# Optimization experiments

Hardware: AMD Instinct MI355X
Metric: run time of the kernel (lower is better)

The kernel has to match this reference:

```python
import jax, jax.numpy as jnp
import numpy as np

DIM = 192; HEADS = 6; WS = 7; RES = 56; SHIFT = 3
HEAD_DIM = DIM // HEADS
SCALE = HEAD_DIM ** -0.5
N = WS * WS
EPS = 1e-5

def _rel_pos_index():
    coords = np.stack(np.meshgrid(np.arange(WS), np.arange(WS), indexing='ij')).reshape(2, -1)
    rel = coords[:, :, None] - coords[:, None, :]  # [2,N,N]
    rel = rel.transpose(1, 2, 0)
    rel[:, :, 0] += WS - 1
    rel[:, :, 1] += WS - 1
    rel[:, :, 0] *= 2 * WS - 1
    return rel.sum(-1)  # [N,N]

def _attn_mask():
    img = np.zeros((RES, RES), dtype=np.float32)
    slices = (slice(0, -WS), slice(-WS, -SHIFT), slice(-SHIFT, None))
    cnt = 0
    for h in slices:
        for w in slices:
            img[h, w] = cnt; cnt += 1
    mw = img.reshape(RES // WS, WS, RES // WS, WS).transpose(0, 2, 1, 3).reshape(-1, N)  # [nW,N]
    diff = mw[:, None, :] - mw[:, :, None]
    return np.where(diff != 0, -100.0, 0.0).astype(np.float32)  # [nW,N,N]

REL_IDX = jnp.asarray(_rel_pos_index())
ATTN_MASK = jnp.asarray(_attn_mask())

def _ln(x, g, b):
    mu = x.mean(-1, keepdims=True)
    var = ((x - mu) ** 2).mean(-1, keepdims=True)
    return (x - mu) * jax.lax.rsqrt(var + EPS) * g + b

def setup_inputs() -> dict:
    key = jax.random.key(0)
    ks = jax.random.split(key, 8)
    d = {
        'x': jax.random.normal(ks[0], (32, RES * RES, DIM), jnp.float32),
        'norm1_g': jnp.ones((DIM,), jnp.float32), 'norm1_b': jnp.zeros((DIM,), jnp.float32),
        'qkv_w': jax.random.normal(ks[1], (DIM, 3 * DIM), jnp.float32) * 0.02,
        'qkv_b': jnp.zeros((3 * DIM,), jnp.float32),
        'proj_w': jax.random.normal(ks[2], (DIM, DIM), jnp.float32) * 0.02,
        'proj_b': jnp.zeros((DIM,), jnp.float32),
        'bias_table': jax.random.normal(ks[3], ((2 * WS - 1) ** 2, HEADS), jnp.float32) * 0.02,
        'norm2_g': jnp.ones((DIM,), jnp.float32), 'norm2_b': jnp.zeros((DIM,), jnp.float32),
        'fc1_w': jax.random.normal(ks[4], (DIM, 4 * DIM), jnp.float32) * 0.02,
        'fc1_b': jnp.zeros((4 * DIM,), jnp.float32),
        'fc2_w': jax.random.normal(ks[5], (4 * DIM, DIM), jnp.float32) * 0.02,
        'fc2_b': jnp.zeros((DIM,), jnp.float32),
    }
    return d

def reference(x, norm1_g, norm1_b, qkv_w, qkv_b, proj_w, proj_b, bias_table,
              norm2_g, norm2_b, fc1_w, fc1_b, fc2_w, fc2_b):
    B, L, C = x.shape
    H = W = RES
    shortcut = x
    h = _ln(x, norm1_g, norm1_b).reshape(B, H, W, C)
    # cyclic shift
    h = jnp.roll(h, (-SHIFT, -SHIFT), axis=(1, 2))
    # window partition -> [B*nW, N, C]
    nH = H // WS
    h = h.reshape(B, nH, WS, nH, WS, C).transpose(0, 1, 3, 2, 4, 5).reshape(-1, N, C)
    BW = h.shape[0]
    # windowed MHSA
    qkv = (h @ qkv_w + qkv_b).reshape(BW, N, 3, HEADS, HEAD_DIM)
    q, k, v = qkv[:, :, 0], qkv[:, :, 1], qkv[:, :, 2]  # [BW,N,h,hd]
    attn = jnp.einsum('bnhd,bmhd->bhnm', q, k) * SCALE  # [BW,h,N,N]
    bias = bias_table[REL_IDX.reshape(-1)].reshape(N, N, HEADS).transpose(2, 0, 1)
    attn = attn + bias[None]
    nW = ATTN_MASK.shape[0]
    attn = attn.reshape(BW // nW, nW, HEADS, N, N) + ATTN_MASK[None, :, None]
    attn = jax.nn.softmax(attn.reshape(BW, HEADS, N, N), axis=-1)
    h = jnp.einsum('bhnm,bmhd->bnhd', attn, v).reshape(BW, N, C)
    h = h @ proj_w + proj_b
    # window reverse
    h = h.reshape(B, nH, nH, WS, WS, C).transpose(0, 1, 3, 2, 4, 5).reshape(B, H, W, C)
    h = jnp.roll(h, (SHIFT, SHIFT), axis=(1, 2)).reshape(B, L, C)
    x = shortcut + h
    # MLP
    m = _ln(x, norm2_g, norm2_b)
    m = jax.nn.gelu(m @ fc1_w + fc1_b, approximate=False) @ fc2_w + fc2_b
    return x + m
```

## Files before the change

kernel.cpp:

```cpp
#include <hip/hip_runtime.h>
#include <hip/hip_bf16.h>
#include <math.h>

typedef __attribute__((ext_vector_type(8))) short bh8;
typedef __attribute__((ext_vector_type(4))) short sh4;
typedef __attribute__((ext_vector_type(4))) float fx4;

__device__ __forceinline__ fx4 mfma_bf16(bh8 a, bh8 b, fx4 c) {
    return __builtin_amdgcn_mfma_f32_16x16x32_bf16(a, b, c, 0, 0, 0);
}

__device__ __forceinline__ void gload16(const __hip_bfloat16* g, __hip_bfloat16* l) {
    __builtin_amdgcn_global_load_lds(
        (const __attribute__((address_space(1))) void*)g,
        (__attribute__((address_space(3))) void*)l,
        16, 0, 0);
}

__device__ __forceinline__ float fast_erf(float u) {
    float au = fabsf(u);
    float t  = __builtin_amdgcn_rcpf(1.0f + 0.3275911f * au);
    float p  = ((((1.061405429f * t - 1.453152027f) * t + 1.421413741f) * t
                 - 0.284496736f) * t + 0.254829592f) * t;
    float e  = __expf(-u * u);
    return copysignf(1.0f - p * e, u);
}

#define WAITV6 do { asm volatile("s_waitcnt vmcnt(6)" ::: "memory"); \
                    __builtin_amdgcn_sched_barrier(0); } while (0)
#define WAITV0 do { asm volatile("s_waitcnt vmcnt(0)" ::: "memory"); \
                    __builtin_amdgcn_sched_barrier(0); } while (0)
#define LGKM0  do { asm volatile("s_waitcnt lgkmcnt(0)" ::: "memory"); \
                    __builtin_amdgcn_sched_barrier(0); } while (0)
#define BARR   do { __builtin_amdgcn_s_barrier(); \
                    __builtin_amdgcn_sched_barrier(0); } while (0)

__global__ __launch_bounds__(256)
void convw_k(const float* __restrict__ W, __hip_bfloat16* __restrict__ Wt, int K, int Nn)
{
    int idx = blockIdx.x * 256 + threadIdx.x;
    if (idx < K * Nn) {
        int k = idx / Nn, n = idx - k * Nn;
        Wt[(size_t)n * K + k] = __float2bfloat16(W[idx]);
    }
}

__global__ __launch_bounds__(256)
void ln1_gather_k(const float* __restrict__ x, const float* __restrict__ g,
                  const float* __restrict__ bia, __hip_bfloat16* __restrict__ xw)
{
    const int wave = threadIdx.x >> 6, lane = threadIdx.x & 63;
    const int t = blockIdx.x * 4 + wave;
    const int w = t / 49, n = t - w * 49;
    const int b = w >> 6, wrem = w & 63, wi = wrem >> 3, wj = wrem & 7;
    const int i = n / 7, j = n - i * 7;
    int sr = wi * 7 + i + 3; if (sr >= 56) sr -= 56;
    int sc = wj * 7 + j + 3; if (sc >= 56) sc -= 56;
    const float* xp = x + ((size_t)b * 3136 + sr * 56 + sc) * 192;
    float v0 = xp[lane], v1 = xp[lane + 64], v2 = xp[lane + 128];
    float s = v0 + v1 + v2;
    float q = v0 * v0 + v1 * v1 + v2 * v2;
    for (int off = 32; off > 0; off >>= 1) {
        s += __shfl_down(s, off, 64);
        q += __shfl_down(q, off, 64);
    }
    s = __shfl(s, 0, 64); q = __shfl(q, 0, 64);
    float mean = s * (1.0f / 192.0f);
    float var  = q * (1.0f / 192.0f) - mean * mean;
    float rstd = rsqrtf(var + 1e-5f);
    __hip_bfloat16* op = xw + (size_t)t * 192;
    op[lane]       = __float2bfloat16((v0 - mean) * rstd * g[lane]       + bia[lane]);
    op[lane + 64]  = __float2bfloat16((v1 - mean) * rstd * g[lane + 64]  + bia[lane + 64]);
    op[lane + 128] = __float2bfloat16((v2 - mean) * rstd * g[lane + 128] + bia[lane + 128]);
}

template<int MODE, int K, int NOUT>
__global__ __launch_bounds__(256)
void gemm2_k(const __hip_bfloat16* __restrict__ A,
             const __hip_bfloat16* __restrict__ Bt,
             const float* __restrict__ bias,
             const float* __restrict__ resid,
             void* __restrict__ outv)
{
    __shared__ __align__(16) __hip_bfloat16 As[128 * 32];
    __shared__ __align__(16) __hip_bfloat16 Bs[64 * 32];
    const int tid  = threadIdx.x;
    const int lane = tid & 63, wave = tid >> 6;
    const int quad = lane >> 4, l15 = lane & 15;
    const int m0 = blockIdx.x * 128, n0 = blockIdx.y * 64;

    const int arow = lane >> 2, acol = (lane & 3) * 8;
    const __hip_bfloat16* Ag0 = A  + (size_t)(m0 + wave * 32 + arow)      * K + acol;
    const __hip_bfloat16* Ag1 = A  + (size_t)(m0 + wave * 32 + 16 + arow) * K + acol;
    const __hip_bfloat16* Bg  = Bt + (size_t)(n0 + wave * 16 + arow)      * K + acol;
    __hip_bfloat16* Al0 = &As[(wave * 32)      * 32];
    __hip_bfloat16* Al1 = &As[(wave * 32 + 16) * 32];
    __hip_bfloat16* Bl  = &Bs[(wave * 16)      * 32];

    fx4 acc[2][4];
#pragma unroll
    for (int mi = 0; mi < 2; mi++)
#pragma unroll
        for (int ni = 0; ni < 4; ni++) acc[mi][ni] = {0.f, 0.f, 0.f, 0.f};

    for (int k0 = 0; k0 < K; k0 += 32) {
        gload16(Ag0 + k0, Al0);
        gload16(Ag1 + k0, Al1);
        gload16(Bg  + k0, Bl);
        __syncthreads();
        bh8 a0 = *(const bh8*)&As[(wave * 32 + l15)      * 32 + quad * 8];
        bh8 a1 = *(const bh8*)&As[(wave * 32 + 16 + l15) * 32 + quad * 8];
        bh8 b0 = *(const bh8*)&Bs[(0 * 16 + l15) * 32 + quad * 8];
        bh8 b1 = *(const bh8*)&Bs[(1 * 16 + l15) * 32 + quad * 8];
        bh8 b2 = *(const bh8*)&Bs[(2 * 16 + l15) * 32 + quad * 8];
        bh8 b3 = *(const bh8*)&Bs[(3 * 16 + l15) * 32 + quad * 8];
        acc[0][0] = mfma_bf16(a0, b0, acc[0][0]);
        acc[0][1] = mfma_bf16(a0, b1, acc[0][1]);
        acc[0][2] = mfma_bf16(a0, b2, acc[0][2]);
        acc[0][3] = mfma_bf16(a0, b3, acc[0][3]);
        acc[1][0] = mfma_bf16(a1, b0, acc[1][0]);
        acc[1][1] = mfma_bf16(a1, b1, acc[1][1]);
        acc[1][2] = mfma_bf16(a1, b2, acc[1][2]);
        acc[1][3] = mfma_bf16(a1, b3, acc[1][3]);
        __syncthreads();
    }

#pragma unroll
    for (int mi = 0; mi < 2; mi++)
#pragma unroll
    for (int ni = 0; ni < 4; ni++) {
        const int n = n0 + ni * 16 + l15;
        const float bn = bias[n];
#pragma unroll
        for (int r = 0; r < 4; r++) {
            const int m = m0 + wave * 32 + mi * 16 + quad * 4 + r;
            float v = acc[mi][ni][r] + bn;
            if (MODE == 0) {
                if (n < 192) v *= 0.17677669529663687f;
                ((__hip_bfloat16*)outv)[(size_t)m * NOUT + n] = __float2bfloat16(v);
            } else if (MODE == 2) {
                v = 0.5f * v * (1.0f + erff(v * 0.70710678118654752f));
                ((__hip_bfloat16*)outv)[(size_t)m * NOUT + n] = __float2bfloat16(v);
            } else {
                ((float*)outv)[(size_t)m * NOUT + n] = v + resid[(size_t)m * NOUT + n];
            }
        }
    }
}

__global__ __launch_bounds__(256, 2)
void mlp_k(const __hip_bfloat16* __restrict__ A,
           const __hip_bfloat16* __restrict__ W1t,
           const __hip_bfloat16* __restrict__ W2t,
           const float* __restrict__ b1,
           const float* __restrict__ b2,
           float* __restrict__ out)
{
    __shared__ __align__(16) __hip_bfloat16 W1s[2][6][32][32];
    __shared__ __align__(16) __hip_bfloat16 W2s[2][192][32];
    __shared__ __align__(16) __hip_bfloat16 Hs[128][40];
    __shared__ __align__(16) float b1s[768];

    const int tid  = threadIdx.x;
    const int lane = tid & 63, wave = tid >> 6;
    const int quad = lane >> 4, l15 = lane & 15;
    const int m0 = blockIdx.x * 128;
    const int arow = lane >> 2, acol = (lane & 3) * 8;

    if (tid < 192) ((fx4*)b1s)[tid] = ((const fx4*)b1)[tid];
    LGKM0;

    bh8 xr[2][6];
    const __hip_bfloat16* xg = A + (size_t)(m0 + wave * 32 + l15) * 192 + quad * 8;
#pragma unroll
    for (int rt = 0; rt < 2; rt++)
#pragma unroll
        for (int kc = 0; kc < 6; kc++)
            xr[rt][kc] = *(const bh8*)(xg + rt * 16 * 192 + kc * 32);

    auto stage = [&](int bf, int c) {
#pragma unroll
        for (int i = 0; i < 3; i++) {
            const int g = wave * 3 + i;
            const int kc = g >> 1, half = g & 1;
            gload16(W1t + (size_t)(c * 32 + half * 16 + arow) * 192 + kc * 32 + acol,
                    &W1s[bf][kc][half * 16][0]);
            gload16(W2t + (size_t)(g * 16 + arow) * 768 + c * 32 + acol,
                    &W2s[bf][g * 16][0]);
        }
    };

    fx4 acc2[2][12];
#pragma unroll
    for (int rt = 0; rt < 2; rt++)
#pragma unroll
        for (int nt = 0; nt < 12; nt++) acc2[rt][nt] = {0.f, 0.f, 0.f, 0.f};

    stage(0, 0);
    stage(1, 1);

    int cur = 0;
    for (int c = 0; c < 23; ++c) {
        WAITV6;
        BARR;

        fx4 bv0 = *(const fx4*)&b1s[c * 32 + 0 * 16 + quad * 4];
        fx4 bv1 = *(const fx4*)&b1s[c * 32 + 1 * 16 + quad * 4];

        fx4 acc1[2][2];
        acc1[0][0] = {0.f, 0.f, 0.f, 0.f}; acc1[0][1] = {0.f, 0.f, 0.f, 0.f};
        acc1[1][0] = {0.f, 0.f, 0.f, 0.f}; acc1[1][1] = {0.f, 0.f, 0.f, 0.f};
        __builtin_amdgcn_s_setprio(1);
#pragma unroll
        for (int kc = 0; kc < 6; kc++) {
#pragma unroll
            for (int ni = 0; ni < 2; ni++) {
                bh8 w = *(const bh8*)&W1s[cur][kc][ni * 16 + l15][quad * 8];
                acc1[0][ni] = mfma_bf16(w, xr[0][kc], acc1[0][ni]);
                acc1[1][ni] = mfma_bf16(w, xr[1][kc], acc1[1][ni]);
            }
        }
        __builtin_amdgcn_s_setprio(0);

#pragma unroll
        for (int rt = 0; rt < 2; rt++) {
#pragma unroll
            for (int ni = 0; ni < 2; ni++) {
                const fx4 bv = ni ? bv1 : bv0;
                sh4 pk;
#pragma unroll
                for (int r = 0; r < 4; r++) {
                    float v = acc1[rt][ni][r] + bv[r];
                    float h = 0.5f * v * (1.0f + fast_erf(v * 0.70710678118654752f));
                    union { __hip_bfloat16 hb; short s; } u;
                    u.hb = __float2bfloat16(h);
                    pk[r] = u.s;
                }
                *(sh4*)&Hs[wave * 32 + rt * 16 + l15][ni * 16 + quad * 4] = pk;
            }
        }
        LGKM0;

        bh8 ha0 = *(const bh8*)&Hs[wave * 32 + l15][quad * 8];
        bh8 ha1 = *(const bh8*)&Hs[wave * 32 + 16 + l15][quad * 8];
        __builtin_amdgcn_s_setprio(1);
#pragma unroll
        for (int nt = 0; nt < 12; nt++) {
            bh8 w2 = *(const bh8*)&W2s[cur][nt * 16 + l15][quad * 8];
            acc2[0][nt] = mfma_bf16(ha0, w2, acc2[0][nt]);
            acc2[1][nt] = mfma_bf16(ha1, w2, acc2[1][nt]);
        }
        __builtin_amdgcn_s_setprio(0);

        BARR;
        if (c < 22) stage(cur, c + 2);
        cur ^= 1;
    }

    {
        WAITV0;
        BARR;
        fx4 bv0 = *(const fx4*)&b1s[23 * 32 + 0 * 16 + quad * 4];
        fx4 bv1 = *(const fx4*)&b1s[23 * 32 + 1 * 16 + quad * 4];
        fx4 acc1[2][2];
        acc1[0][0] = {0.f, 0.f, 0.f, 0.f}; acc1[0][1] = {0.f, 0.f, 0.f, 0.f};
        acc1[1][0] = {0.f, 0.f, 0.f, 0.f}; acc1[1][1] = {0.f, 0.f, 0.f, 0.f};
#pragma unroll
        for (int kc = 0; kc < 6; kc++) {
#pragma unroll
            for (int ni = 0; ni < 2; ni++) {
                bh8 w = *(const bh8*)&W1s[cur][kc][ni * 16 + l15][quad * 8];
                acc1[0][ni] = mfma_bf16(w, xr[0][kc], acc1[0][ni]);
                acc1[1][ni] = mfma_bf16(w, xr[1][kc], acc1[1][ni]);
            }
        }
#pragma unroll
        for (int rt = 0; rt < 2; rt++) {
#pragma unroll
            for (int ni = 0; ni < 2; ni++) {
                const fx4 bv = ni ? bv1 : bv0;
                sh4 pk;
#pragma unroll
                for (int r = 0; r < 4; r++) {
                    float v = acc1[rt][ni][r] + bv[r];
                    float h = 0.5f * v * (1.0f + fast_erf(v * 0.70710678118654752f));
                    union { __hip_bfloat16 hb; short s; } u;
                    u.hb = __float2bfloat16(h);
                    pk[r] = u.s;
                }
                *(sh4*)&Hs[wave * 32 + rt * 16 + l15][ni * 16 + quad * 4] = pk;
            }
        }
        LGKM0;
        bh8 ha0 = *(const bh8*)&Hs[wave * 32 + l15][quad * 8];
        bh8 ha1 = *(const bh8*)&Hs[wave * 32 + 16 + l15][quad * 8];
#pragma unroll
        for (int nt = 0; nt < 12; nt++) {
            bh8 w2 = *(const bh8*)&W2s[cur][nt * 16 + l15][quad * 8];
            acc2[0][nt] = mfma_bf16(ha0, w2, acc2[0][nt]);
            acc2[1][nt] = mfma_bf16(ha1, w2, acc2[1][nt]);
        }
    }

#pragma unroll
    for (int rt = 0; rt < 2; rt++)
#pragma unroll
    for (int nt = 0; nt < 12; nt++) {
        const int n = nt * 16 + l15;
        const float bn = b2[n];
#pragma unroll
        for (int r = 0; r < 4; r++) {
            const int m = m0 + wave * 32 + rt * 16 + quad * 4 + r;
            out[(size_t)m * 192 + n] += acc2[rt][nt][r] + bn;
        }
    }
}

__global__ __launch_bounds__(256)
void projln_k(const __hip_bfloat16* __restrict__ A,
              const __hip_bfloat16* __restrict__ Bt,
              const float* __restrict__ pb,
              const float* __restrict__ xresid,
              const float* __restrict__ g2,
              const float* __restrict__ b2,
              float* __restrict__ x1out,
              __hip_bfloat16* __restrict__ y2out)
{
    __shared__ __align__(16) __hip_bfloat16 As[64 * 32];
    __shared__ __align__(16) __hip_bfloat16 Bs[192 * 32];
    const int tid  = threadIdx.x;
    const int lane = tid & 63, wave = tid >> 6;
    const int quad = lane >> 4, l15 = lane & 15;
    const int m0 = blockIdx.x * 64;

    const int arow = lane >> 2, acol = (lane & 3) * 8;
    const __hip_bfloat16* Ag = A + (size_t)(m0 + wave * 16 + arow) * 192 + acol;
    __hip_bfloat16* Al = &As[(wave * 16) * 32];
    const __hip_bfloat16* Bg0 = Bt + (size_t)((wave + 0) * 16 + arow) * 192 + acol;
    const __hip_bfloat16* Bg1 = Bt + (size_t)((wave + 4) * 16 + arow) * 192 + acol;
    const __hip_bfloat16* Bg2 = Bt + (size_t)((wave + 8) * 16 + arow) * 192 + acol;
    __hip_bfloat16* Bl0 = &Bs[((wave + 0) * 16) * 32];
    __hip_bfloat16* Bl1 = &Bs[((wave + 4) * 16) * 32];
    __hip_bfloat16* Bl2 = &Bs[((wave + 8) * 16) * 32];

    fx4 acc[12];
#pragma unroll
    for (int ct = 0; ct < 12; ct++) acc[ct] = {0.f, 0.f, 0.f, 0.f};

    for (int k0 = 0; k0 < 192; k0 += 32) {
        gload16(Ag  + k0, Al);
        gload16(Bg0 + k0, Bl0);
        gload16(Bg1 + k0, Bl1);
        gload16(Bg2 + k0, Bl2);
        __syncthreads();
        bh8 a = *(const bh8*)&As[(wave * 16 + l15) * 32 + quad * 8];
#pragma unroll
        for (int ct = 0; ct < 12; ct++) {
            bh8 b = *(const bh8*)&Bs[(ct * 16 + l15) * 32 + quad * 8];
            acc[ct] = mfma_bf16(a, b, acc[ct]);
        }
        __syncthreads();
    }

#pragma unroll
    for (int r = 0; r < 4; r++) {
        const int row = m0 + wave * 16 + quad * 4 + r;
        float vv[12];
        float s = 0.f, q = 0.f;
#pragma unroll
        for (int ct = 0; ct < 12; ct++) {
            const int col = ct * 16 + l15;
            float v = acc[ct][r] + pb[col] + xresid[(size_t)row * 192 + col];
            vv[ct] = v;
            x1out[(size_t)row * 192 + col] = v;
            s += v;
            q += v * v;
        }
        s += __shfl_xor(s, 1, 64);  q += __shfl_xor(q, 1, 64);
        s += __shfl_xor(s, 2, 64);  q += __shfl_xor(q, 2, 64);
        s += __shfl_xor(s, 4, 64);  q += __shfl_xor(q, 4, 64);
        s += __shfl_xor(s, 8, 64);  q += __shfl_xor(q, 8, 64);
        float mean = s * (1.0f / 192.0f);
        float var  = q * (1.0f / 192.0f) - mean * mean;
        float rstd = rsqrtf(var + 1e-5f);
#pragma unroll
        for (int ct = 0; ct < 12; ct++) {
            const int col = ct * 16 + l15;
            float y = (vv[ct] - mean) * rstd * g2[col] + b2[col];
            y2out[(size_t)row * 192 + col] = __float2bfloat16(y);
        }
    }
}

__global__ __launch_bounds__(256)
void attn_k(const __hip_bfloat16* __restrict__ qkv,
            const float* __restrict__ bias_table,
            __hip_bfloat16* __restrict__ aout)
{
    __shared__ __align__(16) __hip_bfloat16 Qb[64 * 32];
    __shared__ __align__(16) __hip_bfloat16 Kb[64 * 32];
    __shared__ __align__(16) __hip_bfloat16 Vt[32 * 64];
    __shared__ __align__(16) __hip_bfloat16 Ps[64 * 72];
    __shared__ float bias_h[169];

    const int tid  = threadIdx.x;
    const int lane = tid & 63, wave = tid >> 6;
    const int quad = lane >> 4, l15 = lane & 15;
    const int w = blockIdx.x / 6, hd = blockIdx.x % 6;
    const int b = w >> 6, wrem = w & 63, wi = wrem >> 3, wj = wrem & 7;
    const size_t base = (size_t)w * 49 * 576 + hd * 32;

    if (tid < 169) bias_h[tid] = bias_table[tid * 6 + hd];

    bh8 z = {0, 0, 0, 0, 0, 0, 0, 0};
    {
        int row = tid >> 2, ch = (tid & 3) * 8;
        if (row < 49) {
            *(bh8*)&Qb[row * 32 + ch] = *(const bh8*)(qkv + base + (size_t)row * 576 + ch);
            *(bh8*)&Kb[row * 32 + ch] = *(const bh8*)(qkv + base + (size_t)row * 576 + 192 + ch);
        } else {
            *(bh8*)&Qb[row * 32 + ch] = z;
            *(bh8*)&Kb[row * 32 + ch] = z;
        }
        *(bh8*)&Vt[tid * 8] = z;
    }
    __syncthreads();
    for (int idx = tid; idx < 49 * 32; idx += 256) {
        int n = idx >> 5, d = idx & 31;
        Vt[d * 64 + n] = qkv[base + (size_t)n * 576 + 384 + d];
    }
    __syncthreads();

    fx4 zf = {0.f, 0.f, 0.f, 0.f};
    bh8 aq = *(const bh8*)&Qb[(wave * 16 + l15) * 32 + quad * 8];
    fx4 sarr[4];
#pragma unroll
    for (int ni = 0; ni < 4; ni++) {
        bh8 bk = *(const bh8*)&Kb[(ni * 16 + l15) * 32 + quad * 8];
        sarr[ni] = mfma_bf16(aq, bk, zf);
    }

    int iarr[4], ria[4], cia[4], mbi[4];
#pragma unroll
    for (int r = 0; r < 4; r++) {
        int i = wave * 16 + quad * 4 + r;
        int ri = i / 7, ci = i - ri * 7;
        iarr[r] = i; ria[r] = ri; cia[r] = ci;
        int ar = wi * 7 + ri, ac = wj * 7 + ci;
        int br = (ar < 49) ? 0 : ((ar < 53) ? 1 : 2);
        int bc = (ac < 49) ? 0 : ((ac < 53) ? 1 : 2);
        mbi[r] = br * 3 + bc;
    }
    float vals[4][4];
#pragma unroll
    for (int ni = 0; ni < 4; ni++) {
        int jcol = ni * 16 + l15;
        int rj = jcol / 7, cj = jcol - rj * 7;
        int ar = wi * 7 + rj, ac = wj * 7 + cj;
        int br = (ar < 49) ? 0 : ((ar < 53) ? 1 : 2);
        int bc = (ac < 49) ? 0 : ((ac < 53) ? 1 : 2);
        int mbj = br * 3 + bc;
#pragma unroll
        for (int r = 0; r < 4; r++) {
            float v;
            if (jcol >= 49)            v = -1e30f;
            else if (iarr[r] >= 49)    v = 0.0f;
            else {
                int bidx = (ria[r] - rj + 6) * 13 + (cia[r] - cj + 6);
                v = sarr[ni][r] + bias_h[bidx] + ((mbi[r] != mbj) ? -100.0f : 0.0f);
            }
            vals[ni][r] = v;
        }
    }
#pragma unroll
    for (int r = 0; r < 4; r++) {
        float mx = fmaxf(fmaxf(vals[0][r], vals[1][r]), fmaxf(vals[2][r], vals[3][r]));
        mx = fmaxf(mx, __shfl_xor(mx, 1, 64));
        mx = fmaxf(mx, __shfl_xor(mx, 2, 64));
        mx = fmaxf(mx, __shfl_xor(mx, 4, 64));
        mx = fmaxf(mx, __shfl_xor(mx, 8, 64));
        float e0 = __expf(vals[0][r] - mx);
        float e1 = __expf(vals[1][r] - mx);
        float e2 = __expf(vals[2][r] - mx);
        float e3 = __expf(vals[3][r] - mx);
        float sm = e0 + e1 + e2 + e3;
        sm += __shfl_xor(sm, 1, 64);
        sm += __shfl_xor(sm, 2, 64);
        sm += __shfl_xor(sm, 4, 64);
        sm += __shfl_xor(sm, 8, 64);
        float inv = 1.0f / sm;
        int prow = (wave * 16 + quad * 4 + r) * 72;
        Ps[prow + 0 * 16 + l15] = __float2bfloat16(e0 * inv);
        Ps[prow + 1 * 16 + l15] = __float2bfloat16(e1 * inv);
        Ps[prow + 2 * 16 + l15] = __float2bfloat16(e2 * inv);
        Ps[prow + 3 * 16 + l15] = __float2bfloat16(e3 * inv);
    }
    __syncthreads();

    fx4 o0 = zf, o1 = zf;
#pragma unroll
    for (int k0 = 0; k0 < 64; k0 += 32) {
        bh8 ap  = *(const bh8*)&Ps[(wave * 16 + l15) * 72 + k0 + quad * 8];
        bh8 bv0 = *(const bh8*)&Vt[(l15)      * 64 + k0 + quad * 8];
        bh8 bv1 = *(const bh8*)&Vt[(16 + l15) * 64 + k0 + quad * 8];
        o0 = mfma_bf16(ap, bv0, o0);
        o1 = mfma_bf16(ap, bv1, o1);
    }

#pragma unroll
    for (int r = 0; r < 4; r++) {
        int m = wave * 16 + quad * 4 + r;
        if (m < 49) {
            int i = m / 7, j2 = m - i * 7;
            int orow = wi * 7 + i + 3;  if (orow >= 56) orow -= 56;
            int ocol = wj * 7 + j2 + 3; if (ocol >= 56) ocol -= 56;
            size_t t = (size_t)b * 3136 + orow * 56 + ocol;
            aout[t * 192 + hd * 32 + l15]      = __float2bfloat16(o0[r]);
            aout[t * 192 + hd * 32 + 16 + l15] = __float2bfloat16(o1[r]);
        }
    }
}

extern "C" void kernel_launch(void* const* d_in, const int* in_sizes, int n_in,
                              void* d_out, int out_size, void* d_ws, size_t ws_size,
                              hipStream_t stream)
{
    const float* x      = (const float*)d_in[0];
    const float* n1g    = (const float*)d_in[1];
    const float* n1b    = (const float*)d_in[2];
    const float* qkv_w  = (const float*)d_in[3];
    const float* qkv_b  = (const float*)d_in[4];
    const float* proj_w = (const float*)d_in[5];
    const float* proj_b = (const float*)d_in[6];
    const float* btab   = (const float*)d_in[7];
    const float* n2g    = (const float*)d_in[8];
    const float* n2b    = (const float*)d_in[9];
    const float* fc1_w  = (const float*)d_in[10];
    const float* fc1_b  = (const float*)d_in[11];
    const float* fc2_w  = (const float*)d_in[12];
    const float* fc2_b  = (const float*)d_in[13];

    char* ws = (char*)d_ws;
    __hip_bfloat16* buf1    = (__hip_bfloat16*)(ws + 0);
    __hip_bfloat16* buf2    = (__hip_bfloat16*)(ws + 38535168);
    __hip_bfloat16* wt_qkv  = (__hip_bfloat16*)(ws + 192675840);
    __hip_bfloat16* wt_proj = (__hip_bfloat16*)(ws + 192897024);
    __hip_bfloat16* wt_fc1  = (__hip_bfloat16*)(ws + 192970752);
    __hip_bfloat16* wt_fc2  = (__hip_bfloat16*)(ws + 193265664);
    float*          x1      = (float*)d_out;

    convw_k<<<dim3(432), 256, 0, stream>>>(qkv_w, wt_qkv, 192, 576);
    convw_k<<<dim3(144), 256, 0, stream>>>(proj_w, wt_proj, 192, 192);
    convw_k<<<dim3(576), 256, 0, stream>>>(fc1_w, wt_fc1, 192, 768);
    convw_k<<<dim3(576), 256, 0, stream>>>(fc2_w, wt_fc2, 768, 192);

    ln1_gather_k<<<dim3(25088), 256, 0, stream>>>(x, n1g, n1b, buf1);

    gemm2_k<0, 192, 576><<<dim3(784, 9), 256, 0, stream>>>(buf1, wt_qkv, qkv_b, nullptr, buf2);

    attn_k<<<dim3(12288), 256, 0, stream>>>(buf2, btab, buf1);

    projln_k<<<dim3(1568), 256, 0, stream>>>(buf1, wt_proj, proj_b, x, n2g, n2b, x1, buf1);

    mlp_k<<<dim3(784), 256, 0, stream>>>(buf1, wt_fc1, wt_fc2, fc1_b, fc2_b, x1);
}
```

Measured before the change: 482.7 us.

## Load MLP weight fragments directly from global into registers, dropping LDS staging

The fused MLP kernel no longer double-buffers W1/W2 chunks in shared memory through async global-to-LDS loads with barriers. Each wave now loads its own weight fragments straight from global memory (L2/cache) into registers every chunk, so barriers and LDS traffic go away. The cost is that all four waves fetch the same weights redundantly, global load latency is exposed without a prefetch pipeline, and setprio hints are removed.

```diff
diff --git a/kernel.cpp b/kernel.cpp
--- a/kernel.cpp
+++ b/kernel.cpp
@@ -26,13 +26,7 @@
     return copysignf(1.0f - p * e, u);
 }
 
-#define WAITV6 do { asm volatile("s_waitcnt vmcnt(6)" ::: "memory"); \
-                    __builtin_amdgcn_sched_barrier(0); } while (0)
-#define WAITV0 do { asm volatile("s_waitcnt vmcnt(0)" ::: "memory"); \
-                    __builtin_amdgcn_sched_barrier(0); } while (0)
 #define LGKM0  do { asm volatile("s_waitcnt lgkmcnt(0)" ::: "memory"); \
-                    __builtin_amdgcn_sched_barrier(0); } while (0)
-#define BARR   do { __builtin_amdgcn_s_barrier(); \
                     __builtin_amdgcn_sched_barrier(0); } while (0)
 
 __global__ __launch_bounds__(256)
@@ -156,8 +150,6 @@
            const float* __restrict__ b2,
            float* __restrict__ out)
 {
-    __shared__ __align__(16) __hip_bfloat16 W1s[2][6][32][32];
-    __shared__ __align__(16) __hip_bfloat16 W2s[2][192][32];
     __shared__ __align__(16) __hip_bfloat16 Hs[128][40];
     __shared__ __align__(16) float b1s[768];
 
@@ -165,10 +157,8 @@
     const int lane = tid & 63, wave = tid >> 6;
     const int quad = lane >> 4, l15 = lane & 15;
     const int m0 = blockIdx.x * 128;
-    const int arow = lane >> 2, acol = (lane & 3) * 8;
 
     if (tid < 192) ((fx4*)b1s)[tid] = ((const fx4*)b1)[tid];
-    LGKM0;
 
     bh8 xr[2][6];
     const __hip_bfloat16* xg = A + (size_t)(m0 + wave * 32 + l15) * 192 + quad * 8;
@@ -178,17 +168,10 @@
         for (int kc = 0; kc < 6; kc++)
             xr[rt][kc] = *(const bh8*)(xg + rt * 16 * 192 + kc * 32);
 
-    auto stage = [&](int bf, int c) {
-#pragma unroll
-        for (int i = 0; i < 3; i++) {
-            const int g = wave * 3 + i;
-            const int kc = g >> 1, half = g & 1;
-            gload16(W1t + (size_t)(c * 32 + half * 16 + arow) * 192 + kc * 32 + acol,
-                    &W1s[bf][kc][half * 16][0]);
-            gload16(W2t + (size_t)(g * 16 + arow) * 768 + c * 32 + acol,
-                    &W2s[bf][g * 16][0]);
-        }
-    };
+    __syncthreads();
+
+    const __hip_bfloat16* w1p = W1t + (size_t)l15 * 192 + quad * 8;
+    const __hip_bfloat16* w2p = W2t + (size_t)l15 * 768 + quad * 8;
 
     fx4 acc2[2][12];
 #pragma unroll
@@ -196,31 +179,33 @@
 #pragma unroll
         for (int nt = 0; nt < 12; nt++) acc2[rt][nt] = {0.f, 0.f, 0.f, 0.f};
 
-    stage(0, 0);
-    stage(1, 1);
-
-    int cur = 0;
-    for (int c = 0; c < 23; ++c) {
-        WAITV6;
-        BARR;
-
-        fx4 bv0 = *(const fx4*)&b1s[c * 32 + 0 * 16 + quad * 4];
-        fx4 bv1 = *(const fx4*)&b1s[c * 32 + 1 * 16 + quad * 4];
+    for (int c = 0; c < 24; ++c) {
+        bh8 w1f[6][2];
+#pragma unroll
+        for (int kc = 0; kc < 6; kc++)
+#pragma unroll
+            for (int ni = 0; ni < 2; ni++)
+                w1f[kc][ni] = *(const bh8*)(w1p + (size_t)(c * 32 + ni * 16) * 192
+                                                + kc * 32);
+        fx4 bv0 = *(const fx4*)&b1s[c * 32 + quad * 4];
+        fx4 bv1 = *(const fx4*)&b1s[c * 32 + 16 + quad * 4];
 
         fx4 acc1[2][2];
         acc1[0][0] = {0.f, 0.f, 0.f, 0.f}; acc1[0][1] = {0.f, 0.f, 0.f, 0.f};
         acc1[1][0] = {0.f, 0.f, 0.f, 0.f}; acc1[1][1] = {0.f, 0.f, 0.f, 0.f};
-        __builtin_amdgcn_s_setprio(1);
 #pragma unroll
         for (int kc = 0; kc < 6; kc++) {
 #pragma unroll
             for (int ni = 0; ni < 2; ni++) {
-                bh8 w = *(const bh8*)&W1s[cur][kc][ni * 16 + l15][quad * 8];
-                acc1[0][ni] = mfma_bf16(w, xr[0][kc], acc1[0][ni]);
-                acc1[1][ni] = mfma_bf16(w, xr[1][kc], acc1[1][ni]);
+                acc1[0][ni] = mfma_bf16(w1f[kc][ni], xr[0][kc], acc1[0][ni]);
+                acc1[1][ni] = mfma_bf16(w1f[kc][ni], xr[1][kc], acc1[1][ni]);
             }
         }
-        __builtin_amdgcn_s_setprio(0);
+
+        bh8 w2f[12];
+#pragma unroll
+        for (int nt = 0; nt < 12; nt++)
+            w2f[nt] = *(const bh8*)(w2p + (size_t)nt * 16 * 768 + c * 32);
 
 #pragma unroll
         for (int rt = 0; rt < 2; rt++) {
@@ -243,62 +228,10 @@
 
         bh8 ha0 = *(const bh8*)&Hs[wave * 32 + l15][quad * 8];
         bh8 ha1 = *(const bh8*)&Hs[wave * 32 + 16 + l15][quad * 8];
-        __builtin_amdgcn_s_setprio(1);
 #pragma unroll
         for (int nt = 0; nt < 12; nt++) {
-            bh8 w2 = *(const bh8*)&W2s[cur][nt * 16 + l15][quad * 8];
-            acc2[0][nt] = mfma_bf16(ha0, w2, acc2[0][nt]);
-            acc2[1][nt] = mfma_bf16(ha1, w2, acc2[1][nt]);
-        }
-        __builtin_amdgcn_s_setprio(0);
-
-        BARR;
-        if (c < 22) stage(cur, c + 2);
-        cur ^= 1;
-    }
-
-    {
-        WAITV0;
-        BARR;
-        fx4 bv0 = *(const fx4*)&b1s[23 * 32 + 0 * 16 + quad * 4];
-        fx4 bv1 = *(const fx4*)&b1s[23 * 32 + 1 * 16 + quad * 4];
-        fx4 acc1[2][2];
-        acc1[0][0] = {0.f, 0.f, 0.f, 0.f}; acc1[0][1] = {0.f, 0.f, 0.f, 0.f};
-        acc1[1][0] = {0.f, 0.f, 0.f, 0.f}; acc1[1][1] = {0.f, 0.f, 0.f, 0.f};
-#pragma unroll
-        for (int kc = 0; kc < 6; kc++) {
-#pragma unroll
-            for (int ni = 0; ni < 2; ni++) {
-                bh8 w = *(const bh8*)&W1s[cur][kc][ni * 16 + l15][quad * 8];
-                acc1[0][ni] = mfma_bf16(w, xr[0][kc], acc1[0][ni]);
-                acc1[1][ni] = mfma_bf16(w, xr[1][kc], acc1[1][ni]);
-            }
-        }
-#pragma unroll
-        for (int rt = 0; rt < 2; rt++) {
-#pragma unroll
-            for (int ni = 0; ni < 2; ni++) {
-                const fx4 bv = ni ? bv1 : bv0;
-                sh4 pk;
-#pragma unroll
-                for (int r = 0; r < 4; r++) {
-                    float v = acc1[rt][ni][r] + bv[r];
-                    float h = 0.5f * v * (1.0f + fast_erf(v * 0.70710678118654752f));
-                    union { __hip_bfloat16 hb; short s; } u;
-                    u.hb = __float2bfloat16(h);
-                    pk[r] = u.s;
-                }
-                *(sh4*)&Hs[wave * 32 + rt * 16 + l15][ni * 16 + quad * 4] = pk;
-            }
-        }
-        LGKM0;
-        bh8 ha0 = *(const bh8*)&Hs[wave * 32 + l15][quad * 8];
-        bh8 ha1 = *(const bh8*)&Hs[wave * 32 + 16 + l15][quad * 8];
-#pragma unroll
-        for (int nt = 0; nt < 12; nt++) {
-            bh8 w2 = *(const bh8*)&W2s[cur][nt * 16 + l15][quad * 8];
-            acc2[0][nt] = mfma_bf16(ha0, w2, acc2[0][nt]);
-            acc2[1][nt] = mfma_bf16(ha1, w2, acc2[1][nt]);
+            acc2[0][nt] = mfma_bf16(ha0, w2f[nt], acc2[0][nt]);
+            acc2[1][nt] = mfma_bf16(ha1, w2f[nt], acc2[1][nt]);
         }
     }
 
```

Result: slower. 630.2 us (+30.6%).

## Merge weight conversion launches and remap QKV GEMM block order

Applied to the files above, without the earlier changes.

The four weight-transpose/convert kernels are merged into one launch that branches on a flat index range, cutting three kernel launches. The QKV GEMM drops its unused MODE template branches and moves to a 1D grid whose block index is permuted across groups of 8 (an XCD-aware style swizzle), so neighbouring tiles sharing A rows land on the same chiplet's L2. A bias-load index expression is also simplified without changing its value.

```diff
diff --git a/kernel.cpp b/kernel.cpp
--- a/kernel.cpp
+++ b/kernel.cpp
@@ -36,12 +36,33 @@
                     __builtin_amdgcn_sched_barrier(0); } while (0)
 
 __global__ __launch_bounds__(256)
-void convw_k(const float* __restrict__ W, __hip_bfloat16* __restrict__ Wt, int K, int Nn)
+void convw_all_k(const float* __restrict__ qkv_w, const float* __restrict__ proj_w,
+                 const float* __restrict__ fc1_w, const float* __restrict__ fc2_w,
+                 __hip_bfloat16* __restrict__ wq, __hip_bfloat16* __restrict__ wp,
+                 __hip_bfloat16* __restrict__ w1, __hip_bfloat16* __restrict__ w2)
 {
     int idx = blockIdx.x * 256 + threadIdx.x;
-    if (idx < K * Nn) {
-        int k = idx / Nn, n = idx - k * Nn;
-        Wt[(size_t)n * K + k] = __float2bfloat16(W[idx]);
+    if (idx < 110592) {
+        int k = idx / 576, n = idx - k * 576;
+        wq[(size_t)n * 192 + k] = __float2bfloat16(qkv_w[idx]);
+        return;
+    }
+    idx -= 110592;
+    if (idx < 36864) {
+        int k = idx / 192, n = idx - k * 192;
+        wp[(size_t)n * 192 + k] = __float2bfloat16(proj_w[idx]);
+        return;
+    }
+    idx -= 36864;
+    if (idx < 147456) {
+        int k = idx / 768, n = idx - k * 768;
+        w1[(size_t)n * 192 + k] = __float2bfloat16(fc1_w[idx]);
+        return;
+    }
+    idx -= 147456;
+    if (idx < 147456) {
+        int k = idx / 192, n = idx - k * 192;
+        w2[(size_t)n * 768 + k] = __float2bfloat16(fc2_w[idx]);
     }
 }
 
@@ -74,20 +95,22 @@
     op[lane + 128] = __float2bfloat16((v2 - mean) * rstd * g[lane + 128] + bia[lane + 128]);
 }
 
-template<int MODE, int K, int NOUT>
+template<int K, int NOUT>
 __global__ __launch_bounds__(256)
-void gemm2_k(const __hip_bfloat16* __restrict__ A,
-             const __hip_bfloat16* __restrict__ Bt,
-             const float* __restrict__ bias,
-             const float* __restrict__ resid,
-             void* __restrict__ outv)
+void gemm_qkv_k(const __hip_bfloat16* __restrict__ A,
+                const __hip_bfloat16* __restrict__ Bt,
+                const float* __restrict__ bias,
+                __hip_bfloat16* __restrict__ outv)
 {
     __shared__ __align__(16) __hip_bfloat16 As[128 * 32];
     __shared__ __align__(16) __hip_bfloat16 Bs[64 * 32];
     const int tid  = threadIdx.x;
     const int lane = tid & 63, wave = tid >> 6;
     const int quad = lane >> 4, l15 = lane & 15;
-    const int m0 = blockIdx.x * 128, n0 = blockIdx.y * 64;
+
+    const int nb = NOUT / 64;
+    const int wk = (blockIdx.x & 7) * ((int)gridDim.x >> 3) + ((int)blockIdx.x >> 3);
+    const int m0 = (wk / nb) * 128, n0 = (wk % nb) * 64;
 
     const int arow = lane >> 2, acol = (lane & 3) * 8;
     const __hip_bfloat16* Ag0 = A  + (size_t)(m0 + wave * 32 + arow)      * K + acol;
@@ -135,15 +158,8 @@
         for (int r = 0; r < 4; r++) {
             const int m = m0 + wave * 32 + mi * 16 + quad * 4 + r;
             float v = acc[mi][ni][r] + bn;
-            if (MODE == 0) {
-                if (n < 192) v *= 0.17677669529663687f;
-                ((__hip_bfloat16*)outv)[(size_t)m * NOUT + n] = __float2bfloat16(v);
-            } else if (MODE == 2) {
-                v = 0.5f * v * (1.0f + erff(v * 0.70710678118654752f));
-                ((__hip_bfloat16*)outv)[(size_t)m * NOUT + n] = __float2bfloat16(v);
-            } else {
-                ((float*)outv)[(size_t)m * NOUT + n] = v + resid[(size_t)m * NOUT + n];
-            }
+            if (n < 192) v *= 0.17677669529663687f;
+            outv[(size_t)m * NOUT + n] = __float2bfloat16(v);
         }
     }
 }
@@ -204,8 +220,8 @@
         WAITV6;
         BARR;
 
-        fx4 bv0 = *(const fx4*)&b1s[c * 32 + 0 * 16 + quad * 4];
-        fx4 bv1 = *(const fx4*)&b1s[c * 32 + 1 * 16 + quad * 4];
+        fx4 bv0 = *(const fx4*)&b1s[c * 32 + quad * 4];
+        fx4 bv1 = *(const fx4*)&b1s[c * 32 + 16 + quad * 4];
 
         fx4 acc1[2][2];
         acc1[0][0] = {0.f, 0.f, 0.f, 0.f}; acc1[0][1] = {0.f, 0.f, 0.f, 0.f};
@@ -549,14 +565,12 @@
     __hip_bfloat16* wt_fc2  = (__hip_bfloat16*)(ws + 193265664);
     float*          x1      = (float*)d_out;
 
-    convw_k<<<dim3(432), 256, 0, stream>>>(qkv_w, wt_qkv, 192, 576);
-    convw_k<<<dim3(144), 256, 0, stream>>>(proj_w, wt_proj, 192, 192);
-    convw_k<<<dim3(576), 256, 0, stream>>>(fc1_w, wt_fc1, 192, 768);
-    convw_k<<<dim3(576), 256, 0, stream>>>(fc2_w, wt_fc2, 768, 192);
+    convw_all_k<<<dim3(1728), 256, 0, stream>>>(qkv_w, proj_w, fc1_w, fc2_w,
+                                                wt_qkv, wt_proj, wt_fc1, wt_fc2);
 
     ln1_gather_k<<<dim3(25088), 256, 0, stream>>>(x, n1g, n1b, buf1);
 
-    gemm2_k<0, 192, 576><<<dim3(784, 9), 256, 0, stream>>>(buf1, wt_qkv, qkv_b, nullptr, buf2);
+    gemm_qkv_k<192, 576><<<dim3(7056), 256, 0, stream>>>(buf1, wt_qkv, qkv_b, buf2);
 
     attn_k<<<dim3(12288), 256, 0, stream>>>(buf2, btab, buf1);
 
```

After: 459.8 us. 1.05x faster.
